# Optimization experiments

Measured on AMD Instinct MI355X. Metric: run time of the kernel, lower is better.

## Reference

```python
import jax, jax.numpy as jnp
import numpy as np

N = 10000      # atoms
E = 100000     # edges
C = 64         # hidden channels
S = 16         # spherical harmonic components (l_max=3)
NB = 8         # Bessel basis size
HID = 64       # radial MLP hidden
NE = 10        # chemical elements
G = 64         # graphs in batch
L = 2          # interaction layers
HEADS = 1
RC = 5.0       # radial cutoff
AVG_NEI = 16.0


def _sph_l3(u):
    # real spherical harmonics up to l=3, component normalization, on unit vectors u [E,3]
    x, y, z = u[..., 0], u[..., 1], u[..., 2]
    s3 = 3.0 ** 0.5; s5 = 5.0 ** 0.5; s15 = 15.0 ** 0.5
    c1 = (35.0 / 8.0) ** 0.5; c2 = 105.0 ** 0.5; c3 = (21.0 / 8.0) ** 0.5
    c4 = (7.0 / 4.0) ** 0.5; c5 = (105.0 / 4.0) ** 0.5
    comps = [jnp.ones_like(x),
             s3 * x, s3 * y, s3 * z,
             s15 * x * y, s15 * y * z, (s5 / 2) * (3 * z * z - 1), s15 * x * z, (s15 / 2) * (x * x - y * y),
             c1 * y * (3 * x * x - y * y), c2 * x * y * z, c3 * y * (5 * z * z - 1), c4 * z * (5 * z * z - 3),
             c3 * x * (5 * z * z - 1), c5 * z * (x * x - y * y), c1 * x * (x * x - 3 * y * y)]
    return jnp.stack(comps, axis=-1)  # [E, 16]


def _radial(r):
    # Bessel radial basis * polynomial cutoff (p=6); r [E,1] -> [E, NB]
    n = jnp.arange(1, NB + 1, dtype=r.dtype)
    bessel = (2.0 / RC) ** 0.5 * jnp.sin(n * jnp.pi * r / RC) / r
    t = r / RC
    p = 6.0
    fcut = 1.0 - (p + 1) * (p + 2) / 2 * t ** p + p * (p + 2) * t ** (p + 1) - p * (p + 1) / 2 * t ** (p + 2)
    fcut = jnp.where(r < RC, fcut, 0.0)
    return bessel * fcut


def setup_inputs() -> dict:
    key = jax.random.key(0)
    ks = jax.random.split(key, 20)
    positions = jax.random.uniform(ks[0], (N, 3), dtype=jnp.float32) * 6.0
    species = jax.random.randint(ks[1], (N,), 0, NE)
    node_attrs = jax.nn.one_hot(species, NE, dtype=jnp.float32)
    sender = jax.random.randint(ks[2], (E,), 0, N)
    offs = jax.random.randint(ks[3], (E,), 1, N)
    receiver = (sender + offs) % N  # no self loops
    edge_index = jnp.stack([sender, receiver]).astype(jnp.int32)
    batch = jnp.sort(jax.random.randint(ks[4], (N,), 0, G)).astype(jnp.int32)
    head = jnp.zeros((G,), jnp.int32)
    shifts = jnp.zeros((E, 3), jnp.float32)
    ptr = jnp.arange(G + 1, dtype=jnp.int32)
    w = 0.1
    return {
        'positions': positions, 'node_attrs': node_attrs, 'shifts': shifts,
        'atomic_energies': jax.random.normal(ks[5], (HEADS, NE), jnp.float32),
        'W_emb': w * jax.random.normal(ks[6], (NE, C), jnp.float32),
        'W_up': w * jax.random.normal(ks[7], (L, C, C), jnp.float32),
        'mlp_w1': w * jax.random.normal(ks[8], (L, NB, HID), jnp.float32),
        'mlp_w2': w * jax.random.normal(ks[9], (L, HID, HID), jnp.float32),
        'mlp_w3': w * jax.random.normal(ks[10], (L, HID, C * S), jnp.float32),
        'W_mix': w * jax.random.normal(ks[11], (L, C, C), jnp.float32),
        'W_skip': w * jax.random.normal(ks[12], (L, C, NE, C), jnp.float32),
        'Wc': w * jax.random.normal(ks[13], (L, NE, 3, C), jnp.float32),
        'W_out': w * jax.random.normal(ks[14], (L, C, C), jnp.float32),
        'W_ro': w * jax.random.normal(ks[15], (L, C, HEADS), jnp.float32),
        'edge_index': edge_index, 'batch': batch, 'head': head, 'ptr': ptr,
    }


def reference(positions, node_attrs, shifts, atomic_energies, W_emb, W_up, mlp_w1,
              mlp_w2, mlp_w3, W_mix, W_skip, Wc, W_out, W_ro,
              edge_index, batch, head, ptr):
    n_nodes = positions.shape[0]
    n_graphs = ptr.shape[0] - 1
    sender, receiver = edge_index[0], edge_index[1]
    na = jnp.arange(n_nodes)
    node_heads = head[batch]                                   # [N]
    # isolated-atom reference energies
    node_e0 = (node_attrs @ atomic_energies.T)[na, node_heads]  # [N]
    e0 = jax.ops.segment_sum(node_e0, batch, num_segments=n_graphs)
    node_feats = node_attrs @ W_emb                            # [N, C]
    # edge geometry: gather positions by edge index
    vectors = positions[receiver] - positions[sender] + shifts  # [E, 3]
    lengths = jnp.sqrt(jnp.sum(vectors ** 2, axis=-1, keepdims=True))  # [E, 1]
    edge_attrs = _sph_l3(vectors / lengths)                    # [E, S]
    edge_feats = _radial(lengths)                              # [E, NB]
    energies = [e0, jnp.zeros_like(e0)]  # e0, pair_energy (no pair_repulsion)
    for l in range(W_up.shape[0]):
        # radial MLP -> per-edge tensor-product weights
        h = jax.nn.silu(edge_feats @ mlp_w1[l])
        h = jax.nn.silu(h @ mlp_w2[l])
        tp_w = (h @ mlp_w3[l]).reshape(-1, C, S)               # [E, C, S]
        up = node_feats @ W_up[l]                              # [N, C]
        # gather-compute-scatter message passing
        msg = up[sender][:, :, None] * edge_attrs[:, None, :] * tp_w  # [E, C, S]
        A = jax.ops.segment_sum(msg, receiver, num_segments=n_nodes) / AVG_NEI
        A = jnp.einsum('ncs,cd->nds', A, W_mix[l])             # [N, C, S]
        # element-conditioned skip connection
        sc = jnp.einsum('nc,ced,ne->nd', node_feats, W_skip[l], node_attrs)
        # symmetric-contraction product basis (correlation up to 3), element-conditioned
        w = jnp.einsum('ne,ekc->nkc', node_attrs, Wc[l])       # [N, 3, C]
        p1 = A[:, :, 0]
        p2 = jnp.einsum('ncs,ncs->nc', A, A)
        p3 = p2 * p1
        node_feats = (w[:, 0] * p1 + w[:, 1] * p2 + w[:, 2] * p3) @ W_out[l] + sc
        node_en = (node_feats @ W_ro[l])[na, node_heads]       # [N]
        energies.append(jax.ops.segment_sum(node_en, batch, num_segments=n_graphs))
    contributions = jnp.stack(energies, axis=-1)               # [G, L+2]
    return jnp.sum(contributions, axis=-1)                     # [G]
```

## Files before the change

### kernel.cpp

```cpp
#include <hip/hip_runtime.h>

typedef unsigned short u16;
typedef unsigned int u32;
typedef __attribute__((ext_vector_type(8))) short short8;
typedef __attribute__((ext_vector_type(4))) float f32x4;

#define N_NODES 10000
#define N_EDGES 100000
#define C_CH 64
#define S_SPH 16
#define NB_R 8
#define HID_D 64
#define NE_EL 10
#define G_GR 64
#define L_LAY 2
#define N_HEADS 1
#define RCUT 5.0f
#define INV_AVG (1.0f/16.0f)

__device__ __forceinline__ u16 f2bf(float f) {
  u32 u = __float_as_uint(f);
  u32 r = (u + 0x7FFFu + ((u >> 16) & 1u)) >> 16;
  return (u16)r;
}

__global__ void k_init0(float* __restrict__ out, int* __restrict__ deg) {
  int i = blockIdx.x * 256 + threadIdx.x;
  if (i < G_GR) out[i] = 0.0f;
  if (i < N_NODES) deg[i] = 0;
}

__global__ void k_node_init(const float* __restrict__ attrs, const float* __restrict__ ae,
                            const int* __restrict__ batch, const int* __restrict__ head,
                            int* __restrict__ species, float* __restrict__ out) {
  int n = blockIdx.x * 256 + threadIdx.x;
  if (n >= N_NODES) return;
  int sp = 0;
#pragma unroll
  for (int e = 0; e < NE_EL; ++e)
    if (attrs[n * NE_EL + e] > 0.5f) sp = e;
  species[n] = sp;
  int b = batch[n];
  int h = head[b];
  atomicAdd(&out[b], ae[h * NE_EL + sp]);
}

__global__ void k_embed(const int* __restrict__ species, const float* __restrict__ Wemb,
                        float* __restrict__ feats) {
  int idx = blockIdx.x * 256 + threadIdx.x;
  if (idx >= N_NODES * C_CH) return;
  feats[idx] = Wemb[species[idx >> 6] * C_CH + (idx & 63)];
}

__global__ void k_hist(const int* __restrict__ ei, int* __restrict__ deg) {
  int e = blockIdx.x * 256 + threadIdx.x;
  if (e >= N_EDGES) return;
  atomicAdd(&deg[ei[N_EDGES + e]], 1);
}

__global__ void __launch_bounds__(1024) k_scan(const int* __restrict__ deg,
                                               int* __restrict__ rowptr,
                                               int* __restrict__ woff) {
  __shared__ int wsum[16];
  __shared__ int carry_s;
  int tid = threadIdx.x;
  int lane = tid & 63, w = tid >> 6;
  if (tid == 0) carry_s = 0;
  __syncthreads();
  for (int base = 0; base < N_NODES; base += 1024) {
    int i = base + tid;
    int v = (i < N_NODES) ? deg[i] : 0;
    int orig = v;
#pragma unroll
    for (int off = 1; off < 64; off <<= 1) {
      int n = __shfl_up(v, off, 64);
      if (lane >= off) v += n;
    }
    if (lane == 63) wsum[w] = v;
    __syncthreads();
    if (w == 0 && lane < 16) {
      int x = wsum[lane];
#pragma unroll
      for (int off = 1; off < 16; off <<= 1) {
        int n = __shfl_up(x, off, 16);
        if (lane >= off) x += n;
      }
      wsum[lane] = x;
    }
    __syncthreads();
    int waveoff = (w > 0) ? wsum[w - 1] : 0;
    int carry = carry_s;
    int excl = carry + waveoff + v - orig;
    if (i < N_NODES) {
      rowptr[i] = excl;
      woff[i] = excl;
    }
    int tot = wsum[15];
    __syncthreads();
    if (tid == 0) carry_s = carry + tot;
    __syncthreads();
  }
  if (tid == 0) rowptr[N_NODES] = carry_s;
}

__global__ void k_permute(const int* __restrict__ ei, int* __restrict__ woff,
                          int* __restrict__ rank, int* __restrict__ sndp) {
  int e = blockIdx.x * 256 + threadIdx.x;
  if (e >= N_EDGES) return;
  int rdst = ei[N_EDGES + e];
  int pos = atomicAdd(&woff[rdst], 1);
  rank[e] = pos;
  sndp[pos] = ei[e];
}

__global__ void k_geom(const float* __restrict__ pos, const float* __restrict__ shifts,
                       const int* __restrict__ ei, const int* __restrict__ rank,
                       float* __restrict__ Yp, float* __restrict__ radp) {
  int e = blockIdx.x * 256 + threadIdx.x;
  if (e >= N_EDGES) return;
  int s = ei[e], r = ei[N_EDGES + e];
  float dx = pos[r * 3 + 0] - pos[s * 3 + 0] + shifts[e * 3 + 0];
  float dy = pos[r * 3 + 1] - pos[s * 3 + 1] + shifts[e * 3 + 1];
  float dz = pos[r * 3 + 2] - pos[s * 3 + 2] + shifts[e * 3 + 2];
  float rr = sqrtf(dx * dx + dy * dy + dz * dz);
  rr = fmaxf(rr, 1e-12f);
  float inv = 1.0f / rr;
  float x = dx * inv, y = dy * inv, z = dz * inv;
  float xx = x * x, yy = y * y, zz = z * z;
  const float s3 = 1.73205080757f, s5 = 2.2360679775f, s15 = 3.87298334621f;
  const float c1 = 2.09165006634f, c2 = 10.2469507659f, c3 = 1.62018517461f;
  const float c4 = 1.32287565553f, c5 = 5.12347538298f;
  int rk = rank[e];
  float4* Yo = (float4*)(Yp + (size_t)rk * 16);
  Yo[0] = make_float4(1.0f, s3 * x, s3 * y, s3 * z);
  Yo[1] = make_float4(s15 * x * y, s15 * y * z, 0.5f * s5 * (3.0f * zz - 1.0f), s15 * x * z);
  Yo[2] = make_float4(0.5f * s15 * (xx - yy), c1 * y * (3.0f * xx - yy), c2 * x * y * z,
                      c3 * y * (5.0f * zz - 1.0f));
  Yo[3] = make_float4(c4 * z * (5.0f * zz - 3.0f), c3 * x * (5.0f * zz - 1.0f),
                      c5 * z * (xx - yy), c1 * x * (xx - 3.0f * yy));
  float t = rr * (1.0f / RCUT);
  float t2 = t * t;
  float t6 = t2 * t2 * t2;
  float fcut = 1.0f - 28.0f * t6 + 48.0f * t6 * t - 21.0f * t6 * t2;
  if (rr >= RCUT) fcut = 0.0f;
  float pref = 0.63245553203f * inv * fcut;
  float arg = 3.14159265359f * rr * (1.0f / RCUT);
  float sa, ca;
  __sincosf(arg, &sa, &ca);
  float twoc = 2.0f * ca;
  float sprev = 0.0f, scur = sa;
  float rv[8];
#pragma unroll
  for (int n = 0; n < 8; ++n) {
    rv[n] = pref * scur;
    float snext = twoc * scur - sprev;
    sprev = scur;
    scur = snext;
  }
  float4* Ro = (float4*)(radp + (size_t)rk * 8);
  Ro[0] = make_float4(rv[0], rv[1], rv[2], rv[3]);
  Ro[1] = make_float4(rv[4], rv[5], rv[6], rv[7]);
}

__global__ void k_prep(const float* __restrict__ w3, const float* __restrict__ w2,
                       const float* __restrict__ wmix, u16* __restrict__ w3t,
                       u16* __restrict__ w2t, u16* __restrict__ wmixf) {
  int idx = blockIdx.x * 256 + threadIdx.x;
  if (idx < L_LAY * 65536) {
    int l = idx >> 16;
    int r = idx & 65535;
    int k = r & 63;
    int c = (r >> 6) & 63;
    int s = r >> 12;
    w3t[idx] = f2bf(w3[(l * 64 + k) * 1024 + c * 16 + s]);
  } else if (idx < L_LAY * 65536 + L_LAY * 4096) {
    int i = idx - L_LAY * 65536;
    int l = i >> 12;
    int r = i & 4095;
    int t = r >> 6;
    int j = r & 63;
    w2t[l * 4096 + t * 64 + j] = f2bf(w2[(l * 64 + j) * 64 + t]);
  } else if (idx < L_LAY * 65536 + 2 * L_LAY * 4096) {
    int i = idx - L_LAY * 65536 - L_LAY * 4096;
    int l = i >> 12;
    int r = i & 4095;
    int j = r & 7;
    int col = (r >> 3) & 15;
    int kg = (r >> 7) & 3;
    int hf = (r >> 9) & 1;
    int dc = (r >> 10) & 3;
    int c = hf * 32 + kg * 8 + j;
    int d = dc * 16 + col;
    wmixf[l * 4096 + r] = f2bf(wmix[(l * 64 + c) * 64 + d]);
  }
}

__global__ void __launch_bounds__(64) k_edge_mlp(const float* __restrict__ radp,
                                                 const float* __restrict__ w1,
                                                 const u16* __restrict__ w2T,
                                                 u16* __restrict__ h2) {
  __shared__ float w1s[NB_R * HID_D];
  __shared__ __align__(16) u16 h1b[16 * 64];
  int lane = threadIdx.x;
  for (int i = lane; i < NB_R * HID_D; i += 64) w1s[i] = w1[i];
  int er = lane & 15, jg = lane >> 4;
  int eb = blockIdx.x * 16;
  int e = eb + er;
  float4 ra = *(const float4*)(radp + (size_t)e * 8);
  float4 rb = *(const float4*)(radp + (size_t)e * 8 + 4);
  float rv[8] = {ra.x, ra.y, ra.z, ra.w, rb.x, rb.y, rb.z, rb.w};
  u32* hb = (u32*)h1b;
#pragma unroll
  for (int jj = 0; jj < 16; jj += 2) {
    float p0 = 0.f, p1 = 0.f;
#pragma unroll
    for (int k = 0; k < 8; ++k) {
      p0 += rv[k] * w1s[k * 64 + jg * 16 + jj];
      p1 += rv[k] * w1s[k * 64 + jg * 16 + jj + 1];
    }
    p0 = p0 / (1.f + __expf(-p0));
    p1 = p1 / (1.f + __expf(-p1));
    u32 packed = (u32)f2bf(p0) | ((u32)f2bf(p1) << 16);
    int d = jg * 8 + (jj >> 1);
    hb[er * 32 + (d ^ ((er & 7) << 2))] = packed;
  }
  int row = er, kg = jg, col = er;
  const u32* hbr = (const u32*)h1b;
  short8 a0 = *(const short8*)&hbr[row * 32 + ((kg * 4) ^ ((row & 7) << 2))];
  short8 a1 = *(const short8*)&hbr[row * 32 + ((16 + kg * 4) ^ ((row & 7) << 2))];
#pragma unroll
  for (int ch = 0; ch < 4; ++ch) {
    const u16* wp = w2T + (ch * 16 + col) * 64 + kg * 8;
    short8 b0 = *(const short8*)wp;
    short8 b1 = *(const short8*)(wp + 32);
    f32x4 acc = {0.f, 0.f, 0.f, 0.f};
    acc = __builtin_amdgcn_mfma_f32_16x16x32_bf16(a0, b0, acc, 0, 0, 0);
    acc = __builtin_amdgcn_mfma_f32_16x16x32_bf16(a1, b1, acc, 0, 0, 0);
#pragma unroll
    for (int rr = 0; rr < 4; ++rr) {
      float v = acc[rr];
      v = v / (1.f + __expf(-v));
      h2[(size_t)(eb + kg * 4 + rr) * 64 + ch * 16 + col] = f2bf(v);
    }
  }
}

__global__ void __launch_bounds__(256) k_up(const float* __restrict__ feats,
                                            const float* __restrict__ Wup,
                                            float* __restrict__ up) {
  __shared__ float ws[C_CH * C_CH];
  __shared__ float fs[4][C_CH];
  int tid = threadIdx.x;
  for (int i = tid; i < C_CH * C_CH; i += 256) ws[i] = Wup[i];
  __syncthreads();
  int slot = tid >> 6, t = tid & 63;
  for (int nb = blockIdx.x * 4; nb < N_NODES; nb += gridDim.x * 4) {
    int n = nb + slot;
    fs[slot][t] = feats[n * C_CH + t];
    float acc = 0.0f;
#pragma unroll
    for (int j = 0; j < C_CH; ++j) acc += fs[slot][j] * ws[j * C_CH + t];
    up[n * C_CH + t] = acc * INV_AVG;
  }
}

__global__ void __launch_bounds__(256) k_upe(const float* __restrict__ up,
                                             const int* __restrict__ sndp,
                                             float* __restrict__ upe) {
  int tid = threadIdx.x;
  int slot = tid >> 6, t = tid & 63;
  for (int pb = blockIdx.x * 4; pb < N_EDGES; pb += gridDim.x * 4) {
    int pos = pb + slot;
    upe[(size_t)pos * 64 + t] = up[(size_t)sndp[pos] * 64 + t];
  }
}

__global__ void __launch_bounds__(64) k_gather_fused(
    const u16* __restrict__ h2, const u16* __restrict__ W3T, const float* __restrict__ upe,
    const float* __restrict__ Yp, const int* __restrict__ rowptr,
    const u16* __restrict__ WmixF, const float* __restrict__ featsOld,
    float* __restrict__ featsNew, const float* __restrict__ Wskip,
    const float* __restrict__ Wc, const float* __restrict__ WoutG,
    const float* __restrict__ Wro, const int* __restrict__ species,
    const int* __restrict__ batch, const int* __restrict__ headArr,
    float* __restrict__ out) {
  __shared__ __align__(16) float Yt[16][20];
  __shared__ __align__(16) u16 Asub[4][16][72];
  __shared__ float qs[4][64];
  __shared__ float fsub[4][64];
  int lane = threadIdx.x;
  int row = lane & 15, kg = lane >> 4;
  int col = row;
  int nb = blockIdx.x * 4;
#pragma unroll
  for (int k = 0; k < 4; ++k) fsub[k][lane] = featsOld[(size_t)(nb + k) * 64 + lane];
  int rp0 = rowptr[nb], rp1 = rowptr[nb + 1], rp2 = rowptr[nb + 2], rp3 = rowptr[nb + 3],
      rp4 = rowptr[nb + 4];
  int d0 = rp1 - rp0, d1 = rp2 - rp1, d2 = rp3 - rp2, d3 = rp4 - rp3;
  int rmax = max(max((d0 + 3) >> 2, (d1 + 3) >> 2), max((d2 + 3) >> 2, (d3 + 3) >> 2));
  rmax = max(rmax, 1);
  int nr = row >> 2;
  int baseA = nr == 0 ? rp0 : nr == 1 ? rp1 : nr == 2 ? rp2 : rp3;
  int degA = nr == 0 ? d0 : nr == 1 ? d1 : nr == 2 ? d2 : d3;
  int baseR = kg == 0 ? rp0 : kg == 1 ? rp1 : kg == 2 ? rp2 : rp3;
  int degR = kg == 0 ? d0 : kg == 1 ? d1 : kg == 2 ? d2 : d3;

#pragma unroll 1
  for (int cg = 0; cg < 4; ++cg) {
#pragma unroll 1
    for (int hf = 0; hf < 2; ++hf) {
      short8 B0[8], B1[8];
#pragma unroll
      for (int ss = 0; ss < 8; ++ss) {
        int s = hf * 8 + ss;
        const u16* wp = W3T + (((s * 64 + cg * 16 + col) << 6) + kg * 8);
        B0[ss] = *(const short8*)wp;
        B1[ss] = *(const short8*)(wp + 32);
      }
      float Areg[8];
#pragma unroll
      for (int ss = 0; ss < 8; ++ss) Areg[ss] = 0.f;
#pragma unroll 1
      for (int r = 0; r < rmax; ++r) {
        int sl = r * 4 + (row & 3);
        short8 a0 = {0, 0, 0, 0, 0, 0, 0, 0};
        short8 a1 = {0, 0, 0, 0, 0, 0, 0, 0};
        float4 yq = make_float4(0.f, 0.f, 0.f, 0.f);
        if (sl < degA) {
          int eA = baseA + sl;
          a0 = *(const short8*)(h2 + (size_t)eA * 64 + kg * 8);
          a1 = *(const short8*)(h2 + (size_t)eA * 64 + 32 + kg * 8);
          yq = *(const float4*)(Yp + (size_t)eA * 16 + kg * 4);
        }
        Yt[kg * 4 + 0][row] = yq.x;
        Yt[kg * 4 + 1][row] = yq.y;
        Yt[kg * 4 + 2][row] = yq.z;
        Yt[kg * 4 + 3][row] = yq.w;
        float upv[4];
#pragma unroll
        for (int q = 0; q < 4; ++q) {
          int slq = r * 4 + q;
          int pos = (slq < degR) ? (baseR + slq) : 0;
          float u = upe[(size_t)pos * 64 + cg * 16 + col];
          upv[q] = (slq < degR) ? u : 0.f;
        }
#pragma unroll
        for (int ss = 0; ss < 8; ++ss) {
          f32x4 acc = {0.f, 0.f, 0.f, 0.f};
          acc = __builtin_amdgcn_mfma_f32_16x16x32_bf16(a0, B0[ss], acc, 0, 0, 0);
          acc = __builtin_amdgcn_mfma_f32_16x16x32_bf16(a1, B1[ss], acc, 0, 0, 0);
          float4 yv = *(const float4*)&Yt[hf * 8 + ss][kg * 4];
          Areg[ss] += acc[0] * yv.x * upv[0] + acc[1] * yv.y * upv[1] + acc[2] * yv.z * upv[2] +
                      acc[3] * yv.w * upv[3];
        }
      }
#pragma unroll
      for (int ss = 0; ss < 8; ++ss) Asub[kg][hf * 8 + ss][cg * 16 + col] = f2bf(Areg[ss]);
    }
  }
  __syncthreads();

  short8 WF[4][2];
#pragma unroll
  for (int dc = 0; dc < 4; ++dc)
#pragma unroll
    for (int hf = 0; hf < 2; ++hf)
      WF[dc][hf] = *(const short8*)(WmixF + (size_t)(dc * 1024 + hf * 512 + kg * 128 + row * 8));
  int spArr[4];
#pragma unroll
  for (int k = 0; k < 4; ++k) spArr[k] = species[nb + k];
#pragma unroll 1
  for (int i = 0; i < 4; ++i) {
    short8 a0 = *(const short8*)&Asub[i][row][kg * 8];
    short8 a1 = *(const short8*)&Asub[i][row][32 + kg * 8];
    int sp = spArr[i];
#pragma unroll
    for (int dc = 0; dc < 4; ++dc) {
      f32x4 acc = {0.f, 0.f, 0.f, 0.f};
      acc = __builtin_amdgcn_mfma_f32_16x16x32_bf16(a0, WF[dc][0], acc, 0, 0, 0);
      acc = __builtin_amdgcn_mfma_f32_16x16x32_bf16(a1, WF[dc][1], acc, 0, 0, 0);
      float psq = acc[0] * acc[0] + acc[1] * acc[1] + acc[2] * acc[2] + acc[3] * acc[3];
      psq += __shfl_xor(psq, 16, 64);
      psq += __shfl_xor(psq, 32, 64);
      float p1 = __shfl(acc[0], lane & 15, 64);
      float p3 = psq * p1;
      int d = dc * 16 + row;
      float qv = Wc[(sp * 3 + 0) * 64 + d] * p1 + Wc[(sp * 3 + 1) * 64 + d] * psq +
                 Wc[(sp * 3 + 2) * 64 + d] * p3;
      if (kg == 0) qs[i][d] = qv;
    }
  }
  __syncthreads();

  int t = lane;
  float en[4];
  int bArr[4];
#pragma unroll 1
  for (int i = 0; i < 4; ++i) {
    int sp = spArr[i];
    float sc = 0.f;
#pragma unroll 8
    for (int c = 0; c < 64; ++c) sc += fsub[i][c] * Wskip[(c * NE_EL + sp) * 64 + t];
    float v = sc;
#pragma unroll 8
    for (int d = 0; d < 64; ++d) v += qs[i][d] * WoutG[d * 64 + t];
    featsNew[(size_t)(nb + i) * 64 + t] = v;
    int b = batch[nb + i];
    bArr[i] = b;
    en[i] = v * Wro[t * N_HEADS + headArr[b]];
  }
#pragma unroll
  for (int off = 32; off; off >>= 1) {
#pragma unroll
    for (int i = 0; i < 4; ++i) en[i] += __shfl_down(en[i], off, 64);
  }
  if (lane == 0) {
#pragma unroll
    for (int i = 0; i < 4; ++i) atomicAdd(&out[bArr[i]], en[i]);
  }
}

extern "C" void kernel_launch(void* const* d_in, const int* in_sizes, int n_in,
                              void* d_out, int out_size, void* d_ws, size_t ws_size,
                              hipStream_t stream) {
  const float* pos = (const float*)d_in[0];
  const float* attrs = (const float*)d_in[1];
  const float* shifts = (const float*)d_in[2];
  const float* ae = (const float*)d_in[3];
  const float* Wemb = (const float*)d_in[4];
  const float* Wup = (const float*)d_in[5];
  const float* w1 = (const float*)d_in[6];
  const float* w2 = (const float*)d_in[7];
  const float* w3 = (const float*)d_in[8];
  const float* Wmix = (const float*)d_in[9];
  const float* Wskip = (const float*)d_in[10];
  const float* Wc = (const float*)d_in[11];
  const float* Wout = (const float*)d_in[12];
  const float* Wro = (const float*)d_in[13];
  const int* ei = (const int*)d_in[14];
  const int* batch = (const int*)d_in[15];
  const int* head = (const int*)d_in[16];
  float* out = (float*)d_out;

  char* p = (char*)d_ws;
  float* Yp = (float*)p;     p += (size_t)N_EDGES * 16 * 4;
  float* radp = (float*)p;   p += (size_t)N_EDGES * 8 * 4;
  float* up = (float*)p;     p += (size_t)N_NODES * 64 * 4;
  float* upe = (float*)p;    p += (size_t)N_EDGES * 64 * 4;
  float* fA = (float*)p;     p += (size_t)N_NODES * 64 * 4;
  float* fB = (float*)p;     p += (size_t)N_NODES * 64 * 4;
  u16* h2 = (u16*)p;         p += (size_t)N_EDGES * 64 * 2;
  u16* W3T = (u16*)p;        p += (size_t)L_LAY * 65536 * 2;
  u16* w2T = (u16*)p;        p += (size_t)L_LAY * 4096 * 2;
  u16* WmixF = (u16*)p;      p += (size_t)L_LAY * 4096 * 2;
  int* species = (int*)p;    p += (size_t)N_NODES * 4;
  int* deg = (int*)p;        p += (size_t)N_NODES * 4;
  int* rowptr = (int*)p;     p += (size_t)(N_NODES + 4) * 4;
  int* woff = (int*)p;       p += (size_t)N_NODES * 4;
  int* rank = (int*)p;       p += (size_t)N_EDGES * 4;
  int* sndp = (int*)p;       p += (size_t)N_EDGES * 4;
  if ((size_t)(p - (char*)d_ws) > ws_size) return;

  k_init0<<<(N_NODES + 255) / 256, 256, 0, stream>>>(out, deg);
  k_node_init<<<(N_NODES + 255) / 256, 256, 0, stream>>>(attrs, ae, batch, head, species, out);
  k_embed<<<(N_NODES * C_CH + 255) / 256, 256, 0, stream>>>(species, Wemb, fA);
  k_hist<<<(N_EDGES + 255) / 256, 256, 0, stream>>>(ei, deg);
  k_scan<<<1, 1024, 0, stream>>>(deg, rowptr, woff);
  k_permute<<<(N_EDGES + 255) / 256, 256, 0, stream>>>(ei, woff, rank, sndp);
  k_geom<<<(N_EDGES + 255) / 256, 256, 0, stream>>>(pos, shifts, ei, rank, Yp, radp);
  k_prep<<<(L_LAY * 65536 + 2 * L_LAY * 4096 + 255) / 256, 256, 0, stream>>>(w3, w2, Wmix, W3T,
                                                                             w2T, WmixF);

  const float* fOld = fA;
  float* fNew = fB;
  for (int l = 0; l < L_LAY; ++l) {
    k_edge_mlp<<<N_EDGES / 16, 64, 0, stream>>>(radp, w1 + l * NB_R * HID_D, w2T + l * 4096, h2);
    k_up<<<512, 256, 0, stream>>>(fOld, Wup + l * C_CH * C_CH, up);
    k_upe<<<2048, 256, 0, stream>>>(up, sndp, upe);
    k_gather_fused<<<N_NODES / 4, 64, 0, stream>>>(
        h2, W3T + l * 65536, upe, Yp, rowptr, WmixF + l * 4096, fOld, fNew,
        Wskip + l * C_CH * NE_EL * C_CH, Wc + l * NE_EL * 3 * C_CH, Wout + l * C_CH * C_CH,
        Wro + l * C_CH * N_HEADS, species, batch, head, out);
    const float* tmp = fNew;
    fNew = (float*)fOld;
    fOld = tmp;
  }
}
```

Before: 450.5 us.

## Split fused gather kernel across four waves and software-prefetch edge rows

The fused gather/mix/readout kernel now launches 256 threads per block: each of four waves handles one channel group in the gather phase and one node in the mix and readout phases, where before a single wave looped over all of them serially. The edge-row loop is also software-pipelined, loading h2, Yp and upe for the next row while the MFMAs for the current row run. This adds parallelism per block and hides global load latency. In exchange each wave re-reads the same h2/Yp rows for its channel group, the prefetch raises register pressure, and LDS grows for the per-wave Yt buffers.

```diff
diff --git a/kernel.cpp b/kernel.cpp
--- a/kernel.cpp
+++ b/kernel.cpp
@@ -275,7 +275,7 @@
   }
 }
 
-__global__ void __launch_bounds__(64) k_gather_fused(
+__global__ void __launch_bounds__(256) k_gather_fused(
     const u16* __restrict__ h2, const u16* __restrict__ W3T, const float* __restrict__ upe,
     const float* __restrict__ Yp, const int* __restrict__ rowptr,
     const u16* __restrict__ WmixF, const float* __restrict__ featsOld,
@@ -284,16 +284,18 @@
     const float* __restrict__ Wro, const int* __restrict__ species,
     const int* __restrict__ batch, const int* __restrict__ headArr,
     float* __restrict__ out) {
-  __shared__ __align__(16) float Yt[16][20];
+  __shared__ __align__(16) float Yt[4][16][20];
   __shared__ __align__(16) u16 Asub[4][16][72];
   __shared__ float qs[4][64];
   __shared__ float fsub[4][64];
-  int lane = threadIdx.x;
+  int tid = threadIdx.x;
+  int wv = tid >> 6, lane = tid & 63;
   int row = lane & 15, kg = lane >> 4;
   int col = row;
+  int cg = wv;
+  int cgc = cg * 16 + col;
   int nb = blockIdx.x * 4;
-#pragma unroll
-  for (int k = 0; k < 4; ++k) fsub[k][lane] = featsOld[(size_t)(nb + k) * 64 + lane];
+  fsub[wv][lane] = featsOld[(size_t)(nb + wv) * 64 + lane];
   int rp0 = rowptr[nb], rp1 = rowptr[nb + 1], rp2 = rowptr[nb + 2], rp3 = rowptr[nb + 3],
       rp4 = rowptr[nb + 4];
   int d0 = rp1 - rp0, d1 = rp2 - rp1, d2 = rp3 - rp2, d3 = rp4 - rp3;
@@ -304,120 +306,109 @@
   int degA = nr == 0 ? d0 : nr == 1 ? d1 : nr == 2 ? d2 : d3;
   int baseR = kg == 0 ? rp0 : kg == 1 ? rp1 : kg == 2 ? rp2 : rp3;
   int degR = kg == 0 ? d0 : kg == 1 ? d1 : kg == 2 ? d2 : d3;
+  const short8 z8 = {0, 0, 0, 0, 0, 0, 0, 0};
+
+#define LOADR(RR, A0, A1, YQ, U0, U1, U2, U3)                         \
+  {                                                                   \
+    int sl_ = (RR) * 4 + (row & 3);                                   \
+    if (sl_ < degA) {                                                 \
+      int eA_ = baseA + sl_;                                          \
+      A0 = *(const short8*)(h2 + (size_t)eA_ * 64 + kg * 8);          \
+      A1 = *(const short8*)(h2 + (size_t)eA_ * 64 + 32 + kg * 8);     \
+      YQ = *(const float4*)(Yp + (size_t)eA_ * 16 + kg * 4);          \
+    }                                                                 \
+    int s0_ = (RR) * 4;                                               \
+    int bb_ = baseR + s0_;                                            \
+    U0 = (s0_ + 0 < degR) ? upe[(size_t)(bb_ + 0) * 64 + cgc] : 0.f;  \
+    U1 = (s0_ + 1 < degR) ? upe[(size_t)(bb_ + 1) * 64 + cgc] : 0.f;  \
+    U2 = (s0_ + 2 < degR) ? upe[(size_t)(bb_ + 2) * 64 + cgc] : 0.f;  \
+    U3 = (s0_ + 3 < degR) ? upe[(size_t)(bb_ + 3) * 64 + cgc] : 0.f;  \
+  }
 
 #pragma unroll 1
-  for (int cg = 0; cg < 4; ++cg) {
+  for (int hf = 0; hf < 2; ++hf) {
+    short8 B0[8], B1[8];
+#pragma unroll
+    for (int ss = 0; ss < 8; ++ss) {
+      int s = hf * 8 + ss;
+      const u16* wp = W3T + (((s * 64 + cg * 16 + col) << 6) + kg * 8);
+      B0[ss] = *(const short8*)wp;
+      B1[ss] = *(const short8*)(wp + 32);
+    }
+    float Areg[8];
+#pragma unroll
+    for (int ss = 0; ss < 8; ++ss) Areg[ss] = 0.f;
+    short8 ca0 = z8, ca1 = z8;
+    float4 cyq = make_float4(0.f, 0.f, 0.f, 0.f);
+    float cu0, cu1, cu2, cu3;
+    LOADR(0, ca0, ca1, cyq, cu0, cu1, cu2, cu3);
 #pragma unroll 1
-    for (int hf = 0; hf < 2; ++hf) {
-      short8 B0[8], B1[8];
+    for (int r = 0; r < rmax; ++r) {
+      short8 na0 = z8, na1 = z8;
+      float4 nyq = make_float4(0.f, 0.f, 0.f, 0.f);
+      float nu0 = 0.f, nu1 = 0.f, nu2 = 0.f, nu3 = 0.f;
+      if (r + 1 < rmax) LOADR(r + 1, na0, na1, nyq, nu0, nu1, nu2, nu3);
+      Yt[wv][kg * 4 + 0][row] = cyq.x;
+      Yt[wv][kg * 4 + 1][row] = cyq.y;
+      Yt[wv][kg * 4 + 2][row] = cyq.z;
+      Yt[wv][kg * 4 + 3][row] = cyq.w;
 #pragma unroll
       for (int ss = 0; ss < 8; ++ss) {
-        int s = hf * 8 + ss;
-        const u16* wp = W3T + (((s * 64 + cg * 16 + col) << 6) + kg * 8);
-        B0[ss] = *(const short8*)wp;
-        B1[ss] = *(const short8*)(wp + 32);
+        f32x4 acc = {0.f, 0.f, 0.f, 0.f};
+        acc = __builtin_amdgcn_mfma_f32_16x16x32_bf16(ca0, B0[ss], acc, 0, 0, 0);
+        acc = __builtin_amdgcn_mfma_f32_16x16x32_bf16(ca1, B1[ss], acc, 0, 0, 0);
+        float4 yv = *(const float4*)&Yt[wv][hf * 8 + ss][kg * 4];
+        Areg[ss] += acc[0] * yv.x * cu0 + acc[1] * yv.y * cu1 + acc[2] * yv.z * cu2 +
+                    acc[3] * yv.w * cu3;
       }
-      float Areg[8];
-#pragma unroll
-      for (int ss = 0; ss < 8; ++ss) Areg[ss] = 0.f;
-#pragma unroll 1
-      for (int r = 0; r < rmax; ++r) {
-        int sl = r * 4 + (row & 3);
-        short8 a0 = {0, 0, 0, 0, 0, 0, 0, 0};
-        short8 a1 = {0, 0, 0, 0, 0, 0, 0, 0};
-        float4 yq = make_float4(0.f, 0.f, 0.f, 0.f);
-        if (sl < degA) {
-          int eA = baseA + sl;
-          a0 = *(const short8*)(h2 + (size_t)eA * 64 + kg * 8);
-          a1 = *(const short8*)(h2 + (size_t)eA * 64 + 32 + kg * 8);
-          yq = *(const float4*)(Yp + (size_t)eA * 16 + kg * 4);
-        }
-        Yt[kg * 4 + 0][row] = yq.x;
-        Yt[kg * 4 + 1][row] = yq.y;
-        Yt[kg * 4 + 2][row] = yq.z;
-        Yt[kg * 4 + 3][row] = yq.w;
-        float upv[4];
-#pragma unroll
-        for (int q = 0; q < 4; ++q) {
-          int slq = r * 4 + q;
-          int pos = (slq < degR) ? (baseR + slq) : 0;
-          float u = upe[(size_t)pos * 64 + cg * 16 + col];
-          upv[q] = (slq < degR) ? u : 0.f;
-        }
-#pragma unroll
-        for (int ss = 0; ss < 8; ++ss) {
-          f32x4 acc = {0.f, 0.f, 0.f, 0.f};
-          acc = __builtin_amdgcn_mfma_f32_16x16x32_bf16(a0, B0[ss], acc, 0, 0, 0);
-          acc = __builtin_amdgcn_mfma_f32_16x16x32_bf16(a1, B1[ss], acc, 0, 0, 0);
-          float4 yv = *(const float4*)&Yt[hf * 8 + ss][kg * 4];
-          Areg[ss] += acc[0] * yv.x * upv[0] + acc[1] * yv.y * upv[1] + acc[2] * yv.z * upv[2] +
-                      acc[3] * yv.w * upv[3];
-        }
-      }
-#pragma unroll
-      for (int ss = 0; ss < 8; ++ss) Asub[kg][hf * 8 + ss][cg * 16 + col] = f2bf(Areg[ss]);
-    }
+      ca0 = na0;
+      ca1 = na1;
+      cyq = nyq;
+      cu0 = nu0;
+      cu1 = nu1;
+      cu2 = nu2;
+      cu3 = nu3;
+    }
+#pragma unroll
+    for (int ss = 0; ss < 8; ++ss) Asub[kg][hf * 8 + ss][cg * 16 + col] = f2bf(Areg[ss]);
   }
   __syncthreads();
 
-  short8 WF[4][2];
-#pragma unroll
-  for (int dc = 0; dc < 4; ++dc)
-#pragma unroll
-    for (int hf = 0; hf < 2; ++hf)
-      WF[dc][hf] = *(const short8*)(WmixF + (size_t)(dc * 1024 + hf * 512 + kg * 128 + row * 8));
-  int spArr[4];
-#pragma unroll
-  for (int k = 0; k < 4; ++k) spArr[k] = species[nb + k];
-#pragma unroll 1
-  for (int i = 0; i < 4; ++i) {
-    short8 a0 = *(const short8*)&Asub[i][row][kg * 8];
-    short8 a1 = *(const short8*)&Asub[i][row][32 + kg * 8];
-    int sp = spArr[i];
-#pragma unroll
-    for (int dc = 0; dc < 4; ++dc) {
-      f32x4 acc = {0.f, 0.f, 0.f, 0.f};
-      acc = __builtin_amdgcn_mfma_f32_16x16x32_bf16(a0, WF[dc][0], acc, 0, 0, 0);
-      acc = __builtin_amdgcn_mfma_f32_16x16x32_bf16(a1, WF[dc][1], acc, 0, 0, 0);
-      float psq = acc[0] * acc[0] + acc[1] * acc[1] + acc[2] * acc[2] + acc[3] * acc[3];
-      psq += __shfl_xor(psq, 16, 64);
-      psq += __shfl_xor(psq, 32, 64);
-      float p1 = __shfl(acc[0], lane & 15, 64);
-      float p3 = psq * p1;
-      int d = dc * 16 + row;
-      float qv = Wc[(sp * 3 + 0) * 64 + d] * p1 + Wc[(sp * 3 + 1) * 64 + d] * psq +
-                 Wc[(sp * 3 + 2) * 64 + d] * p3;
-      if (kg == 0) qs[i][d] = qv;
-    }
-  }
-  __syncthreads();
+  int sp = species[nb + wv];
+  short8 a0m = *(const short8*)&Asub[wv][row][kg * 8];
+  short8 a1m = *(const short8*)&Asub[wv][row][32 + kg * 8];
+#pragma unroll
+  for (int dc = 0; dc < 4; ++dc) {
+    short8 wf0 = *(const short8*)(WmixF + (size_t)(dc * 1024 + 0 * 512 + kg * 128 + row * 8));
+    short8 wf1 = *(const short8*)(WmixF + (size_t)(dc * 1024 + 1 * 512 + kg * 128 + row * 8));
+    f32x4 acc = {0.f, 0.f, 0.f, 0.f};
+    acc = __builtin_amdgcn_mfma_f32_16x16x32_bf16(a0m, wf0, acc, 0, 0, 0);
+    acc = __builtin_amdgcn_mfma_f32_16x16x32_bf16(a1m, wf1, acc, 0, 0, 0);
+    float psq = acc[0] * acc[0] + acc[1] * acc[1] + acc[2] * acc[2] + acc[3] * acc[3];
+    psq += __shfl_xor(psq, 16, 64);
+    psq += __shfl_xor(psq, 32, 64);
+    float p1 = __shfl(acc[0], lane & 15, 64);
+    float p3 = psq * p1;
+    int d = dc * 16 + row;
+    float qv = Wc[(sp * 3 + 0) * 64 + d] * p1 + Wc[(sp * 3 + 1) * 64 + d] * psq +
+               Wc[(sp * 3 + 2) * 64 + d] * p3;
+    if (kg == 0) qs[wv][d] = qv;
+  }
 
   int t = lane;
-  float en[4];
-  int bArr[4];
-#pragma unroll 1
-  for (int i = 0; i < 4; ++i) {
-    int sp = spArr[i];
-    float sc = 0.f;
+  float sc = 0.f;
 #pragma unroll 8
-    for (int c = 0; c < 64; ++c) sc += fsub[i][c] * Wskip[(c * NE_EL + sp) * 64 + t];
-    float v = sc;
+  for (int c = 0; c < 64; ++c) sc += fsub[wv][c] * Wskip[(c * NE_EL + sp) * 64 + t];
+  float v = sc;
 #pragma unroll 8
-    for (int d = 0; d < 64; ++d) v += qs[i][d] * WoutG[d * 64 + t];
-    featsNew[(size_t)(nb + i) * 64 + t] = v;
-    int b = batch[nb + i];
-    bArr[i] = b;
-    en[i] = v * Wro[t * N_HEADS + headArr[b]];
-  }
-#pragma unroll
-  for (int off = 32; off; off >>= 1) {
-#pragma unroll
-    for (int i = 0; i < 4; ++i) en[i] += __shfl_down(en[i], off, 64);
-  }
-  if (lane == 0) {
-#pragma unroll
-    for (int i = 0; i < 4; ++i) atomicAdd(&out[bArr[i]], en[i]);
-  }
+  for (int d = 0; d < 64; ++d) v += qs[wv][d] * WoutG[d * 64 + t];
+  featsNew[(size_t)(nb + wv) * 64 + t] = v;
+  int b = batch[nb + wv];
+  float en = v * Wro[t * N_HEADS + headArr[b]];
+#pragma unroll
+  for (int off = 32; off; off >>= 1) en += __shfl_down(en, off, 64);
+  if (lane == 0) atomicAdd(&out[b], en);
+#undef LOADR
 }
 
 extern "C" void kernel_launch(void* const* d_in, const int* in_sizes, int n_in,
@@ -477,7 +468,7 @@
     k_edge_mlp<<<N_EDGES / 16, 64, 0, stream>>>(radp, w1 + l * NB_R * HID_D, w2T + l * 4096, h2);
     k_up<<<512, 256, 0, stream>>>(fOld, Wup + l * C_CH * C_CH, up);
     k_upe<<<2048, 256, 0, stream>>>(up, sndp, upe);
-    k_gather_fused<<<N_NODES / 4, 64, 0, stream>>>(
+    k_gather_fused<<<N_NODES / 4, 256, 0, stream>>>(
         h2, W3T + l * 65536, upe, Yp, rowptr, WmixF + l * 4096, fOld, fNew,
         Wskip + l * C_CH * NE_EL * C_CH, Wc + l * NE_EL * 3 * C_CH, Wout + l * C_CH * C_CH,
         Wro + l * C_CH * N_HEADS, species, batch, head, out);
```

Result: slower. 461.5 us (+2.4%).
